# Optimization experiments

Measured on AMD Instinct MI355X. Metric: run time of the kernel, lower is better.

Reference implementation:

```python
import jax, jax.numpy as jnp
import numpy as np

C = 256
C8 = C // 8

def setup_inputs() -> dict:
    key = jax.random.key(0)
    ks = jax.random.split(key, 7)
    B, H, W = 4, 64, 64
    x = jax.random.normal(ks[0], (B, C, H, W), dtype=jnp.float32)
    s = 1.0 / np.sqrt(C)
    Wq = jax.random.normal(ks[1], (C8, C), dtype=jnp.float32) * s
    bq = jnp.zeros((C8,), dtype=jnp.float32)
    Wk = jax.random.normal(ks[2], (C8, C), dtype=jnp.float32) * s
    bk = jnp.zeros((C8,), dtype=jnp.float32)
    Wv = jax.random.normal(ks[3], (C, C), dtype=jnp.float32) * s
    bv = jnp.zeros((C,), dtype=jnp.float32)
    return {"x": x, "Wq": Wq, "bq": bq, "Wk": Wk, "bk": bk, "Wv": Wv, "bv": bv}

def reference(x, Wq, bq, Wk, bk, Wv, bv):
    B, Cc, H, W = x.shape
    xf = x.reshape(B, Cc, H * W)                      # [B, C, N]
    # 1x1 convs == per-pixel linear projections
    q = jnp.einsum('dc,bcn->bdn', Wq, xf) + bq[None, :, None]   # [B, C/8, N]
    k = jnp.einsum('dc,bcn->bdn', Wk, xf) + bk[None, :, None]   # [B, C/8, N]
    v = jnp.einsum('dc,bcn->bdn', Wv, xf) + bv[None, :, None]   # [B, C,   N]
    scores = jnp.einsum('bdi,bdj->bij', q, k)         # [B, N, N] (no scaling, matching source)
    attn = jax.nn.softmax(scores, axis=-1)
    out = jnp.einsum('bcj,bij->bci', v, attn)         # [B, C, N]
    return out.reshape(B, Cc, H, W) + x
```

## Files before the change

kernel.cpp:

```cpp
#include <hip/hip_runtime.h>
#include <math.h>

#define CCH   256
#define NPIX  4096
#define BATCH 4

typedef __attribute__((ext_vector_type(8))) short    s16x8;
typedef __attribute__((ext_vector_type(4))) short    s16x4;
typedef __attribute__((ext_vector_type(8))) _Float16 f16x8;
typedef __attribute__((ext_vector_type(4))) float    f32x4;

__device__ __forceinline__ unsigned short f2bf(float f) {
    unsigned int u = __float_as_uint(f);
    u += 0x7fff + ((u >> 16) & 1);
    return (unsigned short)(u >> 16);
}
__device__ __forceinline__ float bf2f(unsigned short h) {
    return __uint_as_float(((unsigned int)h) << 16);
}
__device__ __forceinline__ unsigned short f2h(float f) {
    _Float16 h = (_Float16)f;
    return *(unsigned short*)&h;
}
__device__ __forceinline__ float h2f(unsigned short u) {
    _Float16 h = *(_Float16*)&u;
    return (float)h;
}

__device__ __forceinline__ size_t qk_addr(int b, int n, int d) {
    return ((((size_t)b * 256 + (n >> 4)) * 64 + ((d >> 3) << 4) + (n & 15)) << 3) + (d & 7);
}
__device__ __forceinline__ size_t v_addr(int b, int j, int c) {
    return ((((((size_t)b * 64 + (j >> 6)) * 16 + (c >> 4)) * 2 + ((j >> 5) & 1)) * 64
            + (((j >> 3) & 3) << 4) + (c & 15)) << 3) + (j & 7);
}

__global__ __launch_bounds__(64) void wcast_kernel(
    const float* __restrict__ Wq, const float* __restrict__ bq,
    const float* __restrict__ Wk, const float* __restrict__ bk,
    const float* __restrict__ Wv, const float* __restrict__ bv,
    unsigned short* __restrict__ wfh, unsigned short* __restrict__ wfl,
    float* __restrict__ bias_ws)
{
    const int rt = blockIdx.x;
    const int lane = threadIdx.x, l15 = lane & 15, quad = lane >> 4;
    const float *Ws, *bs; int roff; float scale = 1.0f;
    if (rt < 2)      { Ws = Wq; bs = bq; roff = rt * 16;      scale = 1.44269504f; }
    else if (rt < 4) { Ws = Wk; bs = bk; roff = (rt - 2) * 16; }
    else             { Ws = Wv; bs = bv; roff = (rt - 4) * 16; }

    const float* wrow = Ws + (size_t)(roff + l15) * CCH + quad * 8;
    for (int kb = 0; kb < 8; ++kb) {
        s16x8 h, l;
        #pragma unroll
        for (int d = 0; d < 8; ++d) {
            float wv = wrow[kb * 32 + d] * scale;
            unsigned short hh = f2h(wv);
            h[d] = (short)hh;
            l[d] = (short)f2h(wv - h2f(hh));
        }
        *(s16x8*)&wfh[(((size_t)rt * 8 + kb) * 64 + lane) * 8] = h;
        if (rt < 4) *(s16x8*)&wfl[(((size_t)rt * 8 + kb) * 64 + lane) * 8] = l;
    }
    if (lane < 16) bias_ws[rt * 16 + lane] = bs[roff + lane] * scale;
}

__global__ __launch_bounds__(256, 4) void proj_kernel(
    const float* __restrict__ x,
    const unsigned short* __restrict__ wfh, const unsigned short* __restrict__ wfl,
    const float* __restrict__ bias_ws,
    unsigned short* __restrict__ q_hi, unsigned short* __restrict__ k_hi,
    unsigned short* __restrict__ v_frag)
{
    __shared__ float xs[16][260];

    const int t = threadIdx.x;
    const int rh = t >> 6, lane = t & 63, l15 = lane & 15, quad = lane >> 4;
    const int b = blockIdx.y;
    const int nt = blockIdx.x;

    {
        const float* xrow = x + (size_t)b * CCH * NPIX + nt * 16;
        #pragma unroll
        for (int i = 0; i < 4; ++i) {
            const int r  = i * 64 + (t >> 2);
            const int c4 = (t & 3) * 4;
            const float4 v = *(const float4*)&xrow[(size_t)r * NPIX + c4];
            xs[c4 + 0][r] = v.x;
            xs[c4 + 1][r] = v.y;
            xs[c4 + 2][r] = v.z;
            xs[c4 + 3][r] = v.w;
        }
    }
    __syncthreads();

    f32x4 aq0 = {0.f, 0.f, 0.f, 0.f};
    f32x4 aq1 = {0.f, 0.f, 0.f, 0.f};
    f32x4 av[4];
    #pragma unroll
    for (int i = 0; i < 4; ++i) av[i] = (f32x4){0.f, 0.f, 0.f, 0.f};

    #pragma unroll 2
    for (int kb = 0; kb < 8; ++kb) {
        const float4 xv0 = *(const float4*)&xs[l15][kb * 32 + quad * 8];
        const float4 xv1 = *(const float4*)&xs[l15][kb * 32 + quad * 8 + 4];
        const float xa[8] = { xv0.x, xv0.y, xv0.z, xv0.w,
                              xv1.x, xv1.y, xv1.z, xv1.w };
        f16x8 xh, xl;
        #pragma unroll
        for (int d = 0; d < 8; ++d) {
            const float xv = xa[d];
            _Float16 hh = (_Float16)xv;
            xh[d] = hh;
            xl[d] = (_Float16)(xv - (float)hh);
        }
        {
            const f16x8 ah = *(const f16x8*)&wfh[(((size_t)rh * 8 + kb) * 64 + lane) * 8];
            const f16x8 al = *(const f16x8*)&wfl[(((size_t)rh * 8 + kb) * 64 + lane) * 8];
            aq0 = __builtin_amdgcn_mfma_f32_16x16x32_f16(ah, xh, aq0, 0, 0, 0);
            aq1 = __builtin_amdgcn_mfma_f32_16x16x32_f16(ah, xl, aq1, 0, 0, 0);
            aq1 = __builtin_amdgcn_mfma_f32_16x16x32_f16(al, xh, aq1, 0, 0, 0);
        }
        #pragma unroll
        for (int i = 0; i < 4; ++i) {
            const int rt = 4 + rh * 4 + i;
            const f16x8 ah = *(const f16x8*)&wfh[(((size_t)rt * 8 + kb) * 64 + lane) * 8];
            av[i] = __builtin_amdgcn_mfma_f32_16x16x32_f16(ah, xh, av[i], 0, 0, 0);
        }
    }

    const int n = nt * 16 + l15;
    {
        s16x4 h4;
        #pragma unroll
        for (int rr = 0; rr < 4; ++rr) {
            const int rloc = quad * 4 + rr;
            const float val = aq0[rr] + aq1[rr] + bias_ws[rh * 16 + rloc];
            h4[rr] = (short)f2h(val);
        }
        if (rh < 2) {
            const size_t a = qk_addr(b, n, rh * 16 + quad * 4);
            *(s16x4*)&q_hi[a] = h4;
        } else {
            const size_t a = qk_addr(b, n, (rh - 2) * 16 + quad * 4);
            *(s16x4*)&k_hi[a] = h4;
        }
    }
    #pragma unroll
    for (int i = 0; i < 4; ++i) {
        const int vt = rh * 4 + i;
        #pragma unroll
        for (int rr = 0; rr < 4; ++rr) {
            const int rloc = quad * 4 + rr;
            const float val = av[i][rr] + bias_ws[(4 + vt) * 16 + rloc];
            v_frag[v_addr(b, n, vt * 16 + rloc)] = f2bf(val);
        }
    }
}

#define BARRIER_LGKM() do { \
    asm volatile("s_waitcnt lgkmcnt(0)" ::: "memory"); \
    __builtin_amdgcn_s_barrier(); \
    asm volatile("" ::: "memory"); \
} while (0)

#define QK_STEP(KF, BUFC) do { \
    f32x4 a0 = __builtin_amdgcn_mfma_f32_16x16x32_f16((KF), qf0, (f32x4){0.f,0.f,0.f,0.f}, 0, 0, 0); \
    f32x4 a1 = __builtin_amdgcn_mfma_f32_16x16x32_f16((KF), qf1, (f32x4){0.f,0.f,0.f,0.f}, 0, 0, 0); \
    unsigned int u0 = __float_as_uint(__builtin_exp2f(a0[0])) + 0x8000u; \
    unsigned int u1 = __float_as_uint(__builtin_exp2f(a0[1])) + 0x8000u; \
    unsigned int u2 = __float_as_uint(__builtin_exp2f(a0[2])) + 0x8000u; \
    unsigned int u3 = __float_as_uint(__builtin_exp2f(a0[3])) + 0x8000u; \
    uint2 pv; \
    pv.x = __builtin_amdgcn_perm(u1, u0, 0x07060302u); \
    pv.y = __builtin_amdgcn_perm(u3, u2, 0x07060302u); \
    *(uint2*)&p_lds[jh][BUFC][0 * 2 + pfrag_jj][(prow * 16 + l15) * 8 + pcol] = pv; \
    u0 = __float_as_uint(__builtin_exp2f(a1[0])) + 0x8000u; \
    u1 = __float_as_uint(__builtin_exp2f(a1[1])) + 0x8000u; \
    u2 = __float_as_uint(__builtin_exp2f(a1[2])) + 0x8000u; \
    u3 = __float_as_uint(__builtin_exp2f(a1[3])) + 0x8000u; \
    uint2 pw; \
    pw.x = __builtin_amdgcn_perm(u1, u0, 0x07060302u); \
    pw.y = __builtin_amdgcn_perm(u3, u2, 0x07060302u); \
    *(uint2*)&p_lds[jh][BUFC][1 * 2 + pfrag_jj][(prow * 16 + l15) * 8 + pcol] = pw; \
} while (0)

#define ATTN_BODY(T, BUFC, KU, KL, DO_QK) do { \
    const int jt = jh * 32 + (T); \
    const s16x8 pf0 = *(const s16x8*)&p_lds[jh][BUFC][0][lane * 8]; \
    const s16x8 pf1 = *(const s16x8*)&p_lds[jh][BUFC][1][lane * 8]; \
    const s16x8 pf2 = *(const s16x8*)&p_lds[jh][BUFC][2][lane * 8]; \
    const s16x8 pf3 = *(const s16x8*)&p_lds[jh][BUFC][3][lane * 8]; \
    const size_t vbase = (((size_t)jt * 16 + ch * 4) * 2) * 512; \
    const s16x8 v0 = *(const s16x8*)(vb + vbase); \
    const s16x8 v1 = *(const s16x8*)(vb + vbase + 512); \
    const s16x8 v2 = *(const s16x8*)(vb + vbase + 1024); \
    const s16x8 v3 = *(const s16x8*)(vb + vbase + 1536); \
    if (DO_QK) { QK_STEP(KU, (BUFC) ^ 1); } \
    { \
        const int tpp = ((T) + 2 < 32) ? (T) + 2 : 0; \
        const size_t koff = (size_t)((jh * 32 + tpp) * 4 + ch) * 512; \
        KL = *(const f16x8*)(khb + koff); \
    } \
    if (ch == 0) { \
        lacc = __builtin_amdgcn_mfma_f32_16x16x32_bf16(ones, pf0, lacc, 0, 0, 0); \
        lacc = __builtin_amdgcn_mfma_f32_16x16x32_bf16(ones, pf1, lacc, 0, 0, 0); \
    } else if (ch == 1) { \
        lacc = __builtin_amdgcn_mfma_f32_16x16x32_bf16(ones, pf2, lacc, 0, 0, 0); \
        lacc = __builtin_amdgcn_mfma_f32_16x16x32_bf16(ones, pf3, lacc, 0, 0, 0); \
    } \
    BARRIER_LGKM(); \
    const s16x8 v4 = *(const s16x8*)(vb + vbase + 2048); \
    const s16x8 v5 = *(const s16x8*)(vb + vbase + 2560); \
    const s16x8 v6 = *(const s16x8*)(vb + vbase + 3072); \
    const s16x8 v7 = *(const s16x8*)(vb + vbase + 3584); \
    __builtin_amdgcn_s_setprio(1); \
    acc[0] = __builtin_amdgcn_mfma_f32_16x16x32_bf16(v0, pf0, acc[0], 0, 0, 0); \
    acc[0] = __builtin_amdgcn_mfma_f32_16x16x32_bf16(v1, pf1, acc[0], 0, 0, 0); \
    acc[1] = __builtin_amdgcn_mfma_f32_16x16x32_bf16(v0, pf2, acc[1], 0, 0, 0); \
    acc[1] = __builtin_amdgcn_mfma_f32_16x16x32_bf16(v1, pf3, acc[1], 0, 0, 0); \
    acc[2] = __builtin_amdgcn_mfma_f32_16x16x32_bf16(v2, pf0, acc[2], 0, 0, 0); \
    acc[2] = __builtin_amdgcn_mfma_f32_16x16x32_bf16(v3, pf1, acc[2], 0, 0, 0); \
    acc[3] = __builtin_amdgcn_mfma_f32_16x16x32_bf16(v2, pf2, acc[3], 0, 0, 0); \
    acc[3] = __builtin_amdgcn_mfma_f32_16x16x32_bf16(v3, pf3, acc[3], 0, 0, 0); \
    acc[4] = __builtin_amdgcn_mfma_f32_16x16x32_bf16(v4, pf0, acc[4], 0, 0, 0); \
    acc[4] = __builtin_amdgcn_mfma_f32_16x16x32_bf16(v5, pf1, acc[4], 0, 0, 0); \
    acc[5] = __builtin_amdgcn_mfma_f32_16x16x32_bf16(v4, pf2, acc[5], 0, 0, 0); \
    acc[5] = __builtin_amdgcn_mfma_f32_16x16x32_bf16(v5, pf3, acc[5], 0, 0, 0); \
    acc[6] = __builtin_amdgcn_mfma_f32_16x16x32_bf16(v6, pf0, acc[6], 0, 0, 0); \
    acc[6] = __builtin_amdgcn_mfma_f32_16x16x32_bf16(v7, pf1, acc[6], 0, 0, 0); \
    acc[7] = __builtin_amdgcn_mfma_f32_16x16x32_bf16(v6, pf2, acc[7], 0, 0, 0); \
    acc[7] = __builtin_amdgcn_mfma_f32_16x16x32_bf16(v7, pf3, acc[7], 0, 0, 0); \
    __builtin_amdgcn_s_setprio(0); \
} while (0)

__global__ __launch_bounds__(512, 4) void attn_kernel(
    const unsigned short* __restrict__ q_hi,
    const unsigned short* __restrict__ k_hi,
    const unsigned short* __restrict__ v_frag,
    const float* __restrict__ x, float* __restrict__ out)
{
    __shared__ unsigned short p_lds[2][2][4][512];
    __shared__ f32x4 comb[2][4][4][64];
    __shared__ float lds_l[2][2][16];

    const int t = threadIdx.x;
    const int w = t >> 6, lane = t & 63, l15 = lane & 15, quad = lane >> 4;
    const int jh = w >> 2, ch = w & 3;

    const int f = blockIdx.x;
    const int xcd = f & 7;
    const int b = xcd >> 1;
    const int ib = ((xcd & 1) << 6) + (f >> 3);

    f16x8 qf0, qf1;
    {
        const size_t qo0 = ((size_t)b * 256 + ib * 2 + 0) * 512 + (size_t)lane * 8;
        const size_t qo1 = ((size_t)b * 256 + ib * 2 + 1) * 512 + (size_t)lane * 8;
        qf0 = *(const f16x8*)(q_hi + qo0);
        qf1 = *(const f16x8*)(q_hi + qo1);
    }

    const s16x8 ones = { (short)0x3F80, (short)0x3F80, (short)0x3F80, (short)0x3F80,
                         (short)0x3F80, (short)0x3F80, (short)0x3F80, (short)0x3F80 };

    f32x4 acc[8];
    #pragma unroll
    for (int i = 0; i < 8; ++i) acc[i] = (f32x4){0.f, 0.f, 0.f, 0.f};
    f32x4 lacc = {0.f, 0.f, 0.f, 0.f};

    const unsigned short* khb = k_hi + (size_t)b * 131072 + (size_t)lane * 8;
    const unsigned short* vb  = v_frag + (size_t)b * 1048576 + (size_t)lane * 8;

    const int prow = ((ch & 1) << 1) + (quad >> 1);
    const int pcol = ((quad & 1) << 2);
    const int pfrag_jj = ch >> 1;

    f16x8 ka, kb;
    {
        const size_t k0 = (size_t)((jh * 32 + 0) * 4 + ch) * 512;
        ka = *(const f16x8*)(khb + k0);
    }
    QK_STEP(ka, 0);
    {
        const size_t k1 = (size_t)((jh * 32 + 1) * 4 + ch) * 512;
        ka = *(const f16x8*)(khb + k1);
    }
    BARRIER_LGKM();

    #pragma unroll 1
    for (int t2 = 0; t2 < 16; ++t2) {
        ATTN_BODY(2 * t2,     0, ka, kb, 1);
        ATTN_BODY(2 * t2 + 1, 1, kb, ka, (t2 < 15));
    }

    if (ch < 2 && lane < 16) lds_l[jh][ch][lane] = lacc[0];
    if (jh == 0) {
        #pragma unroll
        for (int ct = 0; ct < 4; ++ct)
            comb[0][ch][ct][lane] = acc[ct * 2 + 1];
    } else {
        #pragma unroll
        for (int ct = 0; ct < 4; ++ct)
            comb[1][ch][ct][lane] = acc[ct * 2 + 0];
    }
    __syncthreads();
    const float linv = 1.f / (lds_l[0][jh][l15] + lds_l[1][jh][l15]);
    const int ibase = (ib * 2 + jh) * 16 + l15;
    #pragma unroll
    for (int ct = 0; ct < 4; ++ct) {
        f32x4 a;
        if (jh == 0) a = acc[ct * 2 + 0];
        else         a = acc[ct * 2 + 1];
        a += comb[1 - jh][ch][ct][lane];
        #pragma unroll
        for (int rr = 0; rr < 4; ++rr) {
            const int c = ch * 64 + ct * 16 + quad * 4 + rr;
            const size_t idx = ((size_t)b * CCH + c) * NPIX + ibase;
            out[idx] = a[rr] * linv + x[idx];
        }
    }
}

extern "C" void kernel_launch(void* const* d_in, const int* in_sizes, int n_in,
                              void* d_out, int out_size, void* d_ws, size_t ws_size,
                              hipStream_t stream) {
    const float* x  = (const float*)d_in[0];
    const float* Wq = (const float*)d_in[1];
    const float* bq = (const float*)d_in[2];
    const float* Wk = (const float*)d_in[3];
    const float* bk = (const float*)d_in[4];
    const float* Wv = (const float*)d_in[5];
    const float* bv = (const float*)d_in[6];
    float* out = (float*)d_out;

    unsigned short* ws = (unsigned short*)d_ws;
    unsigned short* q_hi   = ws;
    unsigned short* k_hi   = ws + 1048576;
    unsigned short* v_frag = ws + 2097152;
    unsigned short* wfh    = ws + 6291456;
    unsigned short* wfl    = ws + 6373376;
    float*          bias_ws = (float*)(ws + 6389760);

    wcast_kernel<<<20, 64, 0, stream>>>(Wq, bq, Wk, bk, Wv, bv, wfh, wfl, bias_ws);
    proj_kernel<<<dim3(256, BATCH), 256, 0, stream>>>(x, wfh, wfl, bias_ws,
                                                      q_hi, k_hi, v_frag);
    attn_kernel<<<512, 512, 0, stream>>>(q_hi, k_hi, v_frag, x, out);
}
```

Before: 145.7 us.

## Switch attention to 32x32 MFMA tiles with register-shuffled P

Rewrites the attention kernel to use 32x32x16 MFMA instructions for both QK^T and PV. The exponentiated scores are packed to bf16 with v_cvt_pk_bf16_f32 and rearranged between wave halves with cross-lane shuffles, so the LDS round-trip and per-step barriers for P go away. The Q/K/V fragment layouts are reorganised into 32-wide tiles to match. Each wave now handles its own key range and half of the channels, and the four partial sums are reduced through LDS at the end. This removes the synchronisation in the main loop but uses many more accumulator registers, so the occupancy hint drops from 4 to 2 and the final reduction grows larger.

```diff
diff --git a/kernel.cpp b/kernel.cpp
--- a/kernel.cpp
+++ b/kernel.cpp
@@ -5,10 +5,13 @@
 #define NPIX  4096
 #define BATCH 4
 
-typedef __attribute__((ext_vector_type(8))) short    s16x8;
-typedef __attribute__((ext_vector_type(4))) short    s16x4;
-typedef __attribute__((ext_vector_type(8))) _Float16 f16x8;
-typedef __attribute__((ext_vector_type(4))) float    f32x4;
+typedef __attribute__((ext_vector_type(8)))  short    s16x8;
+typedef __attribute__((ext_vector_type(4)))  short    s16x4;
+typedef __attribute__((ext_vector_type(8)))  _Float16 f16x8;
+typedef __attribute__((ext_vector_type(4)))  float    f32x4;
+typedef __attribute__((ext_vector_type(16))) float    f32x16;
+
+union U8 { unsigned int u[4]; s16x8 v; };
 
 __device__ __forceinline__ unsigned short f2bf(float f) {
     unsigned int u = __float_as_uint(f);
@@ -26,13 +29,19 @@
     _Float16 h = *(_Float16*)&u;
     return (float)h;
 }
-
-__device__ __forceinline__ size_t qk_addr(int b, int n, int d) {
-    return ((((size_t)b * 256 + (n >> 4)) * 64 + ((d >> 3) << 4) + (n & 15)) << 3) + (d & 7);
-}
-__device__ __forceinline__ size_t v_addr(int b, int j, int c) {
-    return ((((((size_t)b * 64 + (j >> 6)) * 16 + (c >> 4)) * 2 + ((j >> 5) & 1)) * 64
-            + (((j >> 3) & 3) << 4) + (c & 15)) << 3) + (j & 7);
+__device__ __forceinline__ unsigned int cvtpk_bf16(float lo, float hi) {
+    unsigned int r;
+    asm("v_cvt_pk_bf16_f32 %0, %1, %2" : "=v"(r) : "v"(lo), "v"(hi));
+    return r;
+}
+
+__device__ __forceinline__ size_t qk_addr32(int b, int n, int d) {
+    return (((((size_t)b * 128 + (n >> 5)) * 2 + (d >> 4)) * 64
+             + (((d >> 3) & 1) << 5) + (n & 31)) << 3) + (d & 7);
+}
+__device__ __forceinline__ size_t v_addr32(int b, int j, int c) {
+    return ((((((size_t)b * 128 + (j >> 5)) * 8 + (c >> 5)) * 2 + ((j >> 4) & 1)) * 64
+             + (((j >> 3) & 1) << 5) + (c & 31)) << 3) + (j & 7);
 }
 
 __global__ __launch_bounds__(64) void wcast_kernel(
@@ -138,13 +147,10 @@
             const float val = aq0[rr] + aq1[rr] + bias_ws[rh * 16 + rloc];
             h4[rr] = (short)f2h(val);
         }
-        if (rh < 2) {
-            const size_t a = qk_addr(b, n, rh * 16 + quad * 4);
-            *(s16x4*)&q_hi[a] = h4;
-        } else {
-            const size_t a = qk_addr(b, n, (rh - 2) * 16 + quad * 4);
-            *(s16x4*)&k_hi[a] = h4;
-        }
+        const int d0 = (rh & 1) * 16 + quad * 4;
+        const size_t a = qk_addr32(b, n, d0);
+        if (rh < 2) *(s16x4*)&q_hi[a] = h4;
+        else        *(s16x4*)&k_hi[a] = h4;
     }
     #pragma unroll
     for (int i = 0; i < 4; ++i) {
@@ -153,171 +159,168 @@
         for (int rr = 0; rr < 4; ++rr) {
             const int rloc = quad * 4 + rr;
             const float val = av[i][rr] + bias_ws[(4 + vt) * 16 + rloc];
-            v_frag[v_addr(b, n, vt * 16 + rloc)] = f2bf(val);
-        }
-    }
-}
-
-#define BARRIER_LGKM() do { \
-    asm volatile("s_waitcnt lgkmcnt(0)" ::: "memory"); \
-    __builtin_amdgcn_s_barrier(); \
-    asm volatile("" ::: "memory"); \
+            v_frag[v_addr32(b, n, vt * 16 + rloc)] = f2bf(val);
+        }
+    }
+}
+
+#define TILE32(JT, KC0, KC1, KN0, KN1, DO_PF) do { \
+    const int jt_ = (JT); \
+    const size_t vb_ = (((size_t)b * 128 + jt_) * 8 + cg * 4) * 1024 + (size_t)lane * 8; \
+    const s16x8 Vf0 = *(const s16x8*)(v_frag + vb_); \
+    const s16x8 Vf1 = *(const s16x8*)(v_frag + vb_ + 512); \
+    const s16x8 Vf2 = *(const s16x8*)(v_frag + vb_ + 1024); \
+    const s16x8 Vf3 = *(const s16x8*)(v_frag + vb_ + 1536); \
+    const s16x8 Vf4 = *(const s16x8*)(v_frag + vb_ + 2048); \
+    const s16x8 Vf5 = *(const s16x8*)(v_frag + vb_ + 2560); \
+    const s16x8 Vf6 = *(const s16x8*)(v_frag + vb_ + 3072); \
+    const s16x8 Vf7 = *(const s16x8*)(v_frag + vb_ + 3584); \
+    f32x16 S = __builtin_amdgcn_mfma_f32_32x32x16_f16((KC0), Q0, \
+        (f32x16){0,0,0,0,0,0,0,0,0,0,0,0,0,0,0,0}, 0, 0, 0); \
+    S = __builtin_amdgcn_mfma_f32_32x32x16_f16((KC1), Q1, S, 0, 0, 0); \
+    if (DO_PF) { \
+        const size_t kb_ = ((size_t)(b * 128 + jt_ + 1) * 2) * 512 + (size_t)lane * 8; \
+        KN0 = *(const f16x8*)(k_hi + kb_); \
+        KN1 = *(const f16x8*)(k_hi + kb_ + 512); \
+    } \
+    const unsigned int pk0 = cvtpk_bf16(__builtin_exp2f(S[0]),  __builtin_exp2f(S[1])); \
+    const unsigned int pk1 = cvtpk_bf16(__builtin_exp2f(S[2]),  __builtin_exp2f(S[3])); \
+    const unsigned int pk2 = cvtpk_bf16(__builtin_exp2f(S[4]),  __builtin_exp2f(S[5])); \
+    const unsigned int pk3 = cvtpk_bf16(__builtin_exp2f(S[6]),  __builtin_exp2f(S[7])); \
+    const unsigned int pk4 = cvtpk_bf16(__builtin_exp2f(S[8]),  __builtin_exp2f(S[9])); \
+    const unsigned int pk5 = cvtpk_bf16(__builtin_exp2f(S[10]), __builtin_exp2f(S[11])); \
+    const unsigned int pk6 = cvtpk_bf16(__builtin_exp2f(S[12]), __builtin_exp2f(S[13])); \
+    const unsigned int pk7 = cvtpk_bf16(__builtin_exp2f(S[14]), __builtin_exp2f(S[15])); \
+    const unsigned int sx0 = (unsigned int)__shfl_xor((int)pk0, 32, 64); \
+    const unsigned int sx1 = (unsigned int)__shfl_xor((int)pk1, 32, 64); \
+    const unsigned int sx2 = (unsigned int)__shfl_xor((int)pk2, 32, 64); \
+    const unsigned int sx3 = (unsigned int)__shfl_xor((int)pk3, 32, 64); \
+    const unsigned int sx4 = (unsigned int)__shfl_xor((int)pk4, 32, 64); \
+    const unsigned int sx5 = (unsigned int)__shfl_xor((int)pk5, 32, 64); \
+    const unsigned int sx6 = (unsigned int)__shfl_xor((int)pk6, 32, 64); \
+    const unsigned int sx7 = (unsigned int)__shfl_xor((int)pk7, 32, 64); \
+    U8 b0_, b1_; \
+    b0_.u[0] = lo_half ? pk0 : sx2;  b0_.u[1] = lo_half ? pk1 : sx3; \
+    b0_.u[2] = lo_half ? sx0 : pk2;  b0_.u[3] = lo_half ? sx1 : pk3; \
+    b1_.u[0] = lo_half ? pk4 : sx6;  b1_.u[1] = lo_half ? pk5 : sx7; \
+    b1_.u[2] = lo_half ? sx4 : pk6;  b1_.u[3] = lo_half ? sx5 : pk7; \
+    const s16x8 B0 = b0_.v, B1 = b1_.v; \
+    dacc = __builtin_amdgcn_mfma_f32_32x32x16_bf16(onesA, B0, dacc, 0, 0, 0); \
+    dacc = __builtin_amdgcn_mfma_f32_32x32x16_bf16(onesA, B1, dacc, 0, 0, 0); \
+    acc0 = __builtin_amdgcn_mfma_f32_32x32x16_bf16(Vf0, B0, acc0, 0, 0, 0); \
+    acc0 = __builtin_amdgcn_mfma_f32_32x32x16_bf16(Vf1, B1, acc0, 0, 0, 0); \
+    acc1 = __builtin_amdgcn_mfma_f32_32x32x16_bf16(Vf2, B0, acc1, 0, 0, 0); \
+    acc1 = __builtin_amdgcn_mfma_f32_32x32x16_bf16(Vf3, B1, acc1, 0, 0, 0); \
+    acc2 = __builtin_amdgcn_mfma_f32_32x32x16_bf16(Vf4, B0, acc2, 0, 0, 0); \
+    acc2 = __builtin_amdgcn_mfma_f32_32x32x16_bf16(Vf5, B1, acc2, 0, 0, 0); \
+    acc3 = __builtin_amdgcn_mfma_f32_32x32x16_bf16(Vf6, B0, acc3, 0, 0, 0); \
+    acc3 = __builtin_amdgcn_mfma_f32_32x32x16_bf16(Vf7, B1, acc3, 0, 0, 0); \
 } while (0)
 
-#define QK_STEP(KF, BUFC) do { \
-    f32x4 a0 = __builtin_amdgcn_mfma_f32_16x16x32_f16((KF), qf0, (f32x4){0.f,0.f,0.f,0.f}, 0, 0, 0); \
-    f32x4 a1 = __builtin_amdgcn_mfma_f32_16x16x32_f16((KF), qf1, (f32x4){0.f,0.f,0.f,0.f}, 0, 0, 0); \
-    unsigned int u0 = __float_as_uint(__builtin_exp2f(a0[0])) + 0x8000u; \
-    unsigned int u1 = __float_as_uint(__builtin_exp2f(a0[1])) + 0x8000u; \
-    unsigned int u2 = __float_as_uint(__builtin_exp2f(a0[2])) + 0x8000u; \
-    unsigned int u3 = __float_as_uint(__builtin_exp2f(a0[3])) + 0x8000u; \
-    uint2 pv; \
-    pv.x = __builtin_amdgcn_perm(u1, u0, 0x07060302u); \
-    pv.y = __builtin_amdgcn_perm(u3, u2, 0x07060302u); \
-    *(uint2*)&p_lds[jh][BUFC][0 * 2 + pfrag_jj][(prow * 16 + l15) * 8 + pcol] = pv; \
-    u0 = __float_as_uint(__builtin_exp2f(a1[0])) + 0x8000u; \
-    u1 = __float_as_uint(__builtin_exp2f(a1[1])) + 0x8000u; \
-    u2 = __float_as_uint(__builtin_exp2f(a1[2])) + 0x8000u; \
-    u3 = __float_as_uint(__builtin_exp2f(a1[3])) + 0x8000u; \
-    uint2 pw; \
-    pw.x = __builtin_amdgcn_perm(u1, u0, 0x07060302u); \
-    pw.y = __builtin_amdgcn_perm(u3, u2, 0x07060302u); \
-    *(uint2*)&p_lds[jh][BUFC][1 * 2 + pfrag_jj][(prow * 16 + l15) * 8 + pcol] = pw; \
-} while (0)
-
-#define ATTN_BODY(T, BUFC, KU, KL, DO_QK) do { \
-    const int jt = jh * 32 + (T); \
-    const s16x8 pf0 = *(const s16x8*)&p_lds[jh][BUFC][0][lane * 8]; \
-    const s16x8 pf1 = *(const s16x8*)&p_lds[jh][BUFC][1][lane * 8]; \
-    const s16x8 pf2 = *(const s16x8*)&p_lds[jh][BUFC][2][lane * 8]; \
-    const s16x8 pf3 = *(const s16x8*)&p_lds[jh][BUFC][3][lane * 8]; \
-    const size_t vbase = (((size_t)jt * 16 + ch * 4) * 2) * 512; \
-    const s16x8 v0 = *(const s16x8*)(vb + vbase); \
-    const s16x8 v1 = *(const s16x8*)(vb + vbase + 512); \
-    const s16x8 v2 = *(const s16x8*)(vb + vbase + 1024); \
-    const s16x8 v3 = *(const s16x8*)(vb + vbase + 1536); \
-    if (DO_QK) { QK_STEP(KU, (BUFC) ^ 1); } \
-    { \
-        const int tpp = ((T) + 2 < 32) ? (T) + 2 : 0; \
-        const size_t koff = (size_t)((jh * 32 + tpp) * 4 + ch) * 512; \
-        KL = *(const f16x8*)(khb + koff); \
-    } \
-    if (ch == 0) { \
-        lacc = __builtin_amdgcn_mfma_f32_16x16x32_bf16(ones, pf0, lacc, 0, 0, 0); \
-        lacc = __builtin_amdgcn_mfma_f32_16x16x32_bf16(ones, pf1, lacc, 0, 0, 0); \
-    } else if (ch == 1) { \
-        lacc = __builtin_amdgcn_mfma_f32_16x16x32_bf16(ones, pf2, lacc, 0, 0, 0); \
-        lacc = __builtin_amdgcn_mfma_f32_16x16x32_bf16(ones, pf3, lacc, 0, 0, 0); \
-    } \
-    BARRIER_LGKM(); \
-    const s16x8 v4 = *(const s16x8*)(vb + vbase + 2048); \
-    const s16x8 v5 = *(const s16x8*)(vb + vbase + 2560); \
-    const s16x8 v6 = *(const s16x8*)(vb + vbase + 3072); \
-    const s16x8 v7 = *(const s16x8*)(vb + vbase + 3584); \
-    __builtin_amdgcn_s_setprio(1); \
-    acc[0] = __builtin_amdgcn_mfma_f32_16x16x32_bf16(v0, pf0, acc[0], 0, 0, 0); \
-    acc[0] = __builtin_amdgcn_mfma_f32_16x16x32_bf16(v1, pf1, acc[0], 0, 0, 0); \
-    acc[1] = __builtin_amdgcn_mfma_f32_16x16x32_bf16(v0, pf2, acc[1], 0, 0, 0); \
-    acc[1] = __builtin_amdgcn_mfma_f32_16x16x32_bf16(v1, pf3, acc[1], 0, 0, 0); \
-    acc[2] = __builtin_amdgcn_mfma_f32_16x16x32_bf16(v2, pf0, acc[2], 0, 0, 0); \
-    acc[2] = __builtin_amdgcn_mfma_f32_16x16x32_bf16(v3, pf1, acc[2], 0, 0, 0); \
-    acc[3] = __builtin_amdgcn_mfma_f32_16x16x32_bf16(v2, pf2, acc[3], 0, 0, 0); \
-    acc[3] = __builtin_amdgcn_mfma_f32_16x16x32_bf16(v3, pf3, acc[3], 0, 0, 0); \
-    acc[4] = __builtin_amdgcn_mfma_f32_16x16x32_bf16(v4, pf0, acc[4], 0, 0, 0); \
-    acc[4] = __builtin_amdgcn_mfma_f32_16x16x32_bf16(v5, pf1, acc[4], 0, 0, 0); \
-    acc[5] = __builtin_amdgcn_mfma_f32_16x16x32_bf16(v4, pf2, acc[5], 0, 0, 0); \
-    acc[5] = __builtin_amdgcn_mfma_f32_16x16x32_bf16(v5, pf3, acc[5], 0, 0, 0); \
-    acc[6] = __builtin_amdgcn_mfma_f32_16x16x32_bf16(v6, pf0, acc[6], 0, 0, 0); \
-    acc[6] = __builtin_amdgcn_mfma_f32_16x16x32_bf16(v7, pf1, acc[6], 0, 0, 0); \
-    acc[7] = __builtin_amdgcn_mfma_f32_16x16x32_bf16(v6, pf2, acc[7], 0, 0, 0); \
-    acc[7] = __builtin_amdgcn_mfma_f32_16x16x32_bf16(v7, pf3, acc[7], 0, 0, 0); \
-    __builtin_amdgcn_s_setprio(0); \
-} while (0)
-
-__global__ __launch_bounds__(512, 4) void attn_kernel(
+__global__ __launch_bounds__(512, 2) void attn_kernel(
     const unsigned short* __restrict__ q_hi,
     const unsigned short* __restrict__ k_hi,
     const unsigned short* __restrict__ v_frag,
     const float* __restrict__ x, float* __restrict__ out)
 {
-    __shared__ unsigned short p_lds[2][2][4][512];
-    __shared__ f32x4 comb[2][4][4][64];
-    __shared__ float lds_l[2][2][16];
+    __shared__ float comb[4][4][16][64];
+    __shared__ float dl[4][32];
 
     const int t = threadIdx.x;
-    const int w = t >> 6, lane = t & 63, l15 = lane & 15, quad = lane >> 4;
-    const int jh = w >> 2, ch = w & 3;
+    const int w = t >> 6, lane = t & 63;
+    const int cg = w & 1, jg = w >> 1;
+    const bool lo_half = (lane < 32);
 
     const int f = blockIdx.x;
     const int xcd = f & 7;
     const int b = xcd >> 1;
     const int ib = ((xcd & 1) << 6) + (f >> 3);
 
-    f16x8 qf0, qf1;
+    const size_t qb = ((size_t)(b * 128 + ib) * 2) * 512 + (size_t)lane * 8;
+    const f16x8 Q0 = *(const f16x8*)(q_hi + qb);
+    const f16x8 Q1 = *(const f16x8*)(q_hi + qb + 512);
+
+    const s16x8 onesA = { (short)0x3F80, (short)0x3F80, (short)0x3F80, (short)0x3F80,
+                          (short)0x3F80, (short)0x3F80, (short)0x3F80, (short)0x3F80 };
+
+    f32x16 acc0 = {0,0,0,0,0,0,0,0,0,0,0,0,0,0,0,0};
+    f32x16 acc1 = {0,0,0,0,0,0,0,0,0,0,0,0,0,0,0,0};
+    f32x16 acc2 = {0,0,0,0,0,0,0,0,0,0,0,0,0,0,0,0};
+    f32x16 acc3 = {0,0,0,0,0,0,0,0,0,0,0,0,0,0,0,0};
+    f32x16 dacc = {0,0,0,0,0,0,0,0,0,0,0,0,0,0,0,0};
+
+    f16x8 kc0, kc1, kn0, kn1;
+    const int jt0 = jg * 32;
     {
-        const size_t qo0 = ((size_t)b * 256 + ib * 2 + 0) * 512 + (size_t)lane * 8;
-        const size_t qo1 = ((size_t)b * 256 + ib * 2 + 1) * 512 + (size_t)lane * 8;
-        qf0 = *(const f16x8*)(q_hi + qo0);
-        qf1 = *(const f16x8*)(q_hi + qo1);
-    }
-
-    const s16x8 ones = { (short)0x3F80, (short)0x3F80, (short)0x3F80, (short)0x3F80,
-                         (short)0x3F80, (short)0x3F80, (short)0x3F80, (short)0x3F80 };
-
-    f32x4 acc[8];
-    #pragma unroll
-    for (int i = 0; i < 8; ++i) acc[i] = (f32x4){0.f, 0.f, 0.f, 0.f};
-    f32x4 lacc = {0.f, 0.f, 0.f, 0.f};
-
-    const unsigned short* khb = k_hi + (size_t)b * 131072 + (size_t)lane * 8;
-    const unsigned short* vb  = v_frag + (size_t)b * 1048576 + (size_t)lane * 8;
-
-    const int prow = ((ch & 1) << 1) + (quad >> 1);
-    const int pcol = ((quad & 1) << 2);
-    const int pfrag_jj = ch >> 1;
-
-    f16x8 ka, kb;
-    {
-        const size_t k0 = (size_t)((jh * 32 + 0) * 4 + ch) * 512;
-        ka = *(const f16x8*)(khb + k0);
-    }
-    QK_STEP(ka, 0);
-    {
-        const size_t k1 = (size_t)((jh * 32 + 1) * 4 + ch) * 512;
-        ka = *(const f16x8*)(khb + k1);
-    }
-    BARRIER_LGKM();
+        const size_t kb0 = ((size_t)(b * 128 + jt0) * 2) * 512 + (size_t)lane * 8;
+        kc0 = *(const f16x8*)(k_hi + kb0);
+        kc1 = *(const f16x8*)(k_hi + kb0 + 512);
+    }
+    kn0 = kc0; kn1 = kc1;
 
     #pragma unroll 1
-    for (int t2 = 0; t2 < 16; ++t2) {
-        ATTN_BODY(2 * t2,     0, ka, kb, 1);
-        ATTN_BODY(2 * t2 + 1, 1, kb, ka, (t2 < 15));
-    }
-
-    if (ch < 2 && lane < 16) lds_l[jh][ch][lane] = lacc[0];
-    if (jh == 0) {
-        #pragma unroll
-        for (int ct = 0; ct < 4; ++ct)
-            comb[0][ch][ct][lane] = acc[ct * 2 + 1];
-    } else {
-        #pragma unroll
-        for (int ct = 0; ct < 4; ++ct)
-            comb[1][ch][ct][lane] = acc[ct * 2 + 0];
+    for (int s2 = 0; s2 < 16; ++s2) {
+        TILE32(jt0 + 2 * s2,     kc0, kc1, kn0, kn1, 1);
+        TILE32(jt0 + 2 * s2 + 1, kn0, kn1, kc0, kc1, (s2 < 15));
+    }
+
+    if (cg == 0 && lane < 32) dl[jg][lane] = dacc[0];
+    if (jg & 1) {
+        const int slot = cg * 2 + (jg >> 1);
+        #pragma unroll
+        for (int r = 0; r < 16; ++r) {
+            comb[slot][0][r][lane] = acc0[r];
+            comb[slot][1][r][lane] = acc1[r];
+            comb[slot][2][r][lane] = acc2[r];
+            comb[slot][3][r][lane] = acc3[r];
+        }
     }
     __syncthreads();
-    const float linv = 1.f / (lds_l[0][jh][l15] + lds_l[1][jh][l15]);
-    const int ibase = (ib * 2 + jh) * 16 + l15;
-    #pragma unroll
-    for (int ct = 0; ct < 4; ++ct) {
-        f32x4 a;
-        if (jh == 0) a = acc[ct * 2 + 0];
-        else         a = acc[ct * 2 + 1];
-        a += comb[1 - jh][ch][ct][lane];
-        #pragma unroll
-        for (int rr = 0; rr < 4; ++rr) {
-            const int c = ch * 64 + ct * 16 + quad * 4 + rr;
-            const size_t idx = ((size_t)b * CCH + c) * NPIX + ibase;
-            out[idx] = a[rr] * linv + x[idx];
+    if (!(jg & 1)) {
+        const int slot = cg * 2 + (jg >> 1);
+        #pragma unroll
+        for (int r = 0; r < 16; ++r) {
+            acc0[r] += comb[slot][0][r][lane];
+            acc1[r] += comb[slot][1][r][lane];
+            acc2[r] += comb[slot][2][r][lane];
+            acc3[r] += comb[slot][3][r][lane];
+        }
+    }
+    __syncthreads();
+    if (jg == 2) {
+        #pragma unroll
+        for (int r = 0; r < 16; ++r) {
+            comb[cg * 2][0][r][lane] = acc0[r];
+            comb[cg * 2][1][r][lane] = acc1[r];
+            comb[cg * 2][2][r][lane] = acc2[r];
+            comb[cg * 2][3][r][lane] = acc3[r];
+        }
+    }
+    __syncthreads();
+    if (jg == 0) {
+        #pragma unroll
+        for (int r = 0; r < 16; ++r) {
+            acc0[r] += comb[cg * 2][0][r][lane];
+            acc1[r] += comb[cg * 2][1][r][lane];
+            acc2[r] += comb[cg * 2][2][r][lane];
+            acc3[r] += comb[cg * 2][3][r][lane];
+        }
+        const int l31 = lane & 31;
+        const float linv = 1.f / (dl[0][l31] + dl[1][l31] + dl[2][l31] + dl[3][l31]);
+        const int ipix = ib * 32 + l31;
+        const int rplus = (lane >> 5) << 2;
+        const size_t obase = ((size_t)b * CCH + cg * 128) * NPIX + ipix;
+        #pragma unroll
+        for (int r = 0; r < 16; ++r) {
+            const int crow = (r & 3) + ((r >> 2) << 3) + rplus;
+            const size_t i0 = obase + (size_t)(crow +  0) * NPIX;
+            const size_t i1 = obase + (size_t)(crow + 32) * NPIX;
+            const size_t i2 = obase + (size_t)(crow + 64) * NPIX;
+            const size_t i3 = obase + (size_t)(crow + 96) * NPIX;
+            out[i0] = acc0[r] * linv + x[i0];
+            out[i1] = acc1[r] * linv + x[i1];
+            out[i2] = acc2[r] * linv + x[i2];
+            out[i3] = acc3[r] * linv + x[i3];
         }
     }
 }
```

New measurement: 169.1 us. 16.1% more time.
